# Kernel optimization log

Hardware: AMD Instinct MI355X
Metric: run time of the kernel (lower is better)

Reference implementation:

```python
import jax, jax.numpy as jnp
import numpy as np


def _conv1x1(w, x):
    # w: [out, in], x: [B, in, H, W] -> [B, out, H, W]
    return jnp.einsum('oc,bchw->bohw', w, x)


def _maxpool2(x):
    # 2x2 max pool, stride 2. x: [B, C, H, W] -> [B, C, H//2, W//2]
    B, C, H, W = x.shape
    return x.reshape(B, C, H // 2, 2, W // 2, 2).max(axis=(3, 5))


def setup_inputs() -> dict:
    key = jax.random.key(0)
    ks = jax.random.split(key, 5)
    B, C, H, W = 8, 256, 64, 64
    div = 8
    x = jax.random.normal(ks[0], (B, C, H, W), dtype=jnp.float32)
    wq = jax.random.normal(ks[1], (C // div, C), dtype=jnp.float32) * (C ** -0.5)
    wk = jax.random.normal(ks[2], (C // div, C), dtype=jnp.float32) * (C ** -0.5)
    wv = jax.random.normal(ks[3], (C // 2, C), dtype=jnp.float32) * (C ** -0.5)
    wo = jax.random.normal(ks[4], (C, C // 2), dtype=jnp.float32) * ((C // 2) ** -0.5)
    gamma = jnp.float32(0.5)  # nonzero so attention branch contributes
    return {"x": x, "wq": wq, "wk": wk, "wv": wv, "wo": wo, "gamma": gamma}


def reference(x, wq, wk, wv, wo, gamma):
    B, C, H, W = x.shape
    HW = H * W
    # query: [B, HW, Cq]
    q = _conv1x1(wq, x).reshape(B, -1, HW).transpose(0, 2, 1)
    # key: maxpool -> [B, Cq, HW//4]
    k = _maxpool2(_conv1x1(wk, x)).reshape(B, -1, HW // 4)
    # value: maxpool -> [B, C//2, HW//4]
    v = _maxpool2(_conv1x1(wv, x)).reshape(B, -1, HW // 4)
    scores = jnp.einsum('bnc,bcm->bnm', q, k)          # [B, HW, HW//4]
    attn = jax.nn.softmax(scores, axis=2)
    ctx = jnp.einsum('bcm,bnm->bcn', v, attn)          # [B, C//2, HW]
    ctx = ctx.reshape(B, C // 2, H, W)
    out = gamma * _conv1x1(wo, ctx) + x
    return out
```

## Files before the change

kernel.cpp:

```cpp
#include <hip/hip_runtime.h>
#include <hip/hip_bf16.h>

#define BB  8
#define CC  256
#define HW  4096
#define CQ  32
#define CV  128
#define MP  1024

#define XT_OFF  0
#define Y_OFF   4194304
#define KT_OFF  (Y_OFF + 3145728)
#define VP_OFF  (KT_OFF + 131072)
#define CT_OFF  (VP_OFF + 524288)
#define P0_OFF  CT_OFF
#define P1_OFF  XT_OFF
#define ML_OFF  (XT_OFF + 2097152)

typedef __attribute__((ext_vector_type(8))) short bf16x8;
typedef __attribute__((ext_vector_type(4))) short short4v;
typedef __attribute__((ext_vector_type(4))) float f32x4;

__device__ __forceinline__ short f2b(float f) {
    unsigned u = __float_as_uint(f);
    u += 0x7fffu + ((u >> 16) & 1u);
    return (short)(u >> 16);
}
__device__ __forceinline__ float b2f(short s) {
    return __uint_as_float(((unsigned)(unsigned short)s) << 16);
}

__global__ __launch_bounds__(256) void k_xt(
    const float* __restrict__ x, short* __restrict__ xt)
{
    __shared__ float t[64][65];
    const int bid = blockIdx.x;
    const int nt = bid & 63;
    const int ct = (bid >> 6) & 3;
    const int b  = bid >> 8;
    const int c0 = ct * 64, n0 = nt * 64;
    const int tid = threadIdx.x;

    const int col = tid & 63, wrow = (tid >> 6) * 16;
    #pragma unroll
    for (int i = 0; i < 16; ++i) {
        int r = wrow + i;
        t[r][col] = x[((long)(b * CC + c0 + r)) * HW + n0 + col];
    }
    __syncthreads();

    const int n = tid >> 2, cb = (tid & 3) * 16;
    short buf[16];
    #pragma unroll
    for (int j = 0; j < 16; ++j) buf[j] = f2b(t[cb + j][n]);
    short* dst = &xt[((long)(b * HW + n0 + n)) * CC + c0 + cb];
    *(int4*)dst = *(int4*)&buf[0];
    *(int4*)(dst + 8) = *(int4*)&buf[8];
}

__global__ __launch_bounds__(256) void k_qkv(
    const float* __restrict__ wq, const float* __restrict__ wk,
    const float* __restrict__ wv, const short* __restrict__ xt,
    short* __restrict__ y)
{
    __shared__ short w_lds[96 * 264];
    __shared__ short x_lds[256 * 40];
    const int bid = blockIdx.x;
    const int oc = bid & 1;
    const int nt = (bid >> 1) & 15;
    const int b  = bid >> 5;
    const int o0 = oc * 96, n0 = nt * 256;
    const int tid = threadIdx.x;
    const int lane = tid & 63;
    const int wvid = tid >> 6;
    const int l15 = lane & 15, g = lane >> 4;

    for (int it = 0; it < 24; ++it) {
        int idx = tid + it * 256;
        int ol = idx >> 6, cq = (idx & 63) * 4;
        int o = o0 + ol;
        const float* src = (o < 32) ? &wq[o * 256 + cq]
                         : (o < 64) ? &wk[(o - 32) * 256 + cq]
                                    : &wv[(o - 64) * 256 + cq];
        float4 w = *(const float4*)src;
        short4v p = { f2b(w.x), f2b(w.y), f2b(w.z), f2b(w.w) };
        *(short4v*)&w_lds[ol * 264 + cq] = p;
    }

    f32x4 acc[4][6];
    #pragma unroll
    for (int nf = 0; nf < 4; ++nf)
        #pragma unroll
        for (int of = 0; of < 6; ++of) acc[nf][of] = (f32x4){0.f, 0.f, 0.f, 0.f};

    for (int ks = 0; ks < 8; ++ks) {
        __syncthreads();
        {
            const short* src = &xt[((long)(b * HW + n0 + tid)) * CC + ks * 32];
            int4 v0 = *(const int4*)src;
            int4 v1 = *(const int4*)(src + 8);
            int4 v2 = *(const int4*)(src + 16);
            int4 v3 = *(const int4*)(src + 24);
            short* dst = &x_lds[tid * 40];
            *(int4*)dst = v0; *(int4*)(dst + 8) = v1;
            *(int4*)(dst + 16) = v2; *(int4*)(dst + 24) = v3;
        }
        __syncthreads();

        bf16x8 a[4], bf[6];
        #pragma unroll
        for (int nf = 0; nf < 4; ++nf)
            a[nf] = *(const bf16x8*)&x_lds[(wvid * 64 + nf * 16 + l15) * 40 + 8 * g];
        #pragma unroll
        for (int of = 0; of < 6; ++of)
            bf[of] = *(const bf16x8*)&w_lds[(of * 16 + l15) * 264 + ks * 32 + 8 * g];
        #pragma unroll
        for (int nf = 0; nf < 4; ++nf)
            #pragma unroll
            for (int of = 0; of < 6; ++of)
                acc[nf][of] = __builtin_amdgcn_mfma_f32_16x16x32_bf16(a[nf], bf[of], acc[nf][of], 0, 0, 0);
    }

    #pragma unroll
    for (int nf = 0; nf < 4; ++nf) {
        #pragma unroll
        for (int of = 0; of < 6; ++of) {
            int o = o0 + of * 16 + l15;
            long nb = (long)(b * HW + n0 + wvid * 64 + nf * 16 + 4 * g);
            #pragma unroll
            for (int r = 0; r < 4; ++r)
                y[(nb + r) * 192 + o] = f2b(acc[nf][of][r]);
        }
    }
}

__global__ __launch_bounds__(256) void k_pool(
    const short* __restrict__ y, short* __restrict__ kT, short* __restrict__ vp)
{
    __shared__ short t[64 * 136];
    const int bid = blockIdx.x;
    const int mt = bid & 15;
    const int b  = bid >> 4;
    const int m0 = mt * 64;
    const int tid = threadIdx.x;

    {
        int ml = tid >> 2, ci = (tid & 3) * 8;
        int pp = m0 + ml;
        int ph = pp >> 5, pw = pp & 31;
        const short* src = &y[((long)(b * HW) + ph * 128 + pw * 2) * 192 + 32 + ci];
        int4 s0 = *(const int4*)src;
        int4 s1 = *(const int4*)(src + 192);
        int4 s2 = *(const int4*)(src + 12288);
        int4 s3 = *(const int4*)(src + 12480);
        const short *a = (const short*)&s0, *bb = (const short*)&s1,
                    *c = (const short*)&s2, *d = (const short*)&s3;
        short o8[8];
        #pragma unroll
        for (int j = 0; j < 8; ++j)
            o8[j] = f2b(fmaxf(fmaxf(b2f(a[j]), b2f(bb[j])), fmaxf(b2f(c[j]), b2f(d[j]))));
        *(int4*)&kT[((long)(b * MP + pp)) * CQ + ci] = *(int4*)o8;
    }
    #pragma unroll
    for (int jj = 0; jj < 4; ++jj) {
        int idx = tid + jj * 256;
        int ml = idx >> 4, ci = (idx & 15) * 8;
        int pp = m0 + ml;
        int ph = pp >> 5, pw = pp & 31;
        const short* src = &y[((long)(b * HW) + ph * 128 + pw * 2) * 192 + 64 + ci];
        int4 s0 = *(const int4*)src;
        int4 s1 = *(const int4*)(src + 192);
        int4 s2 = *(const int4*)(src + 12288);
        int4 s3 = *(const int4*)(src + 12480);
        const short *a = (const short*)&s0, *bb = (const short*)&s1,
                    *c = (const short*)&s2, *d = (const short*)&s3;
        short o8[8];
        #pragma unroll
        for (int j = 0; j < 8; ++j)
            o8[j] = f2b(fmaxf(fmaxf(b2f(a[j]), b2f(bb[j])), fmaxf(b2f(c[j]), b2f(d[j]))));
        *(int4*)&t[ml * 136 + ci] = *(int4*)o8;
    }
    __syncthreads();
    {
        int c = tid & 127, mc = (tid >> 7) * 32;
        short buf[32];
        #pragma unroll
        for (int mm = 0; mm < 32; ++mm) buf[mm] = t[(mc + mm) * 136 + c];
        short* dst = &vp[((long)(b * CV + c)) * MP + m0 + mc];
        *(int4*)dst = *(int4*)&buf[0];
        *(int4*)(dst + 8)  = *(int4*)&buf[8];
        *(int4*)(dst + 16) = *(int4*)&buf[16];
        *(int4*)(dst + 24) = *(int4*)&buf[24];
    }
}

__global__ __launch_bounds__(128) void k_attn(
    const short* __restrict__ y,
    const short* __restrict__ kT,
    const short* __restrict__ vp,
    short* __restrict__ p0,
    short* __restrict__ p1,
    float* __restrict__ ml)
{
    __shared__ short p_lds[2][2][16][40];
    const int tid   = threadIdx.x;
    const int lane  = tid & 63;
    const int wid   = tid >> 6;
    const int split = blockIdx.x >> 9;
    const int rem   = blockIdx.x & 511;
    const int b     = rem >> 6;
    const int q0    = (rem & 63) * 64 + wid * 32;
    const int l15   = lane & 15;
    const int g     = lane >> 4;

    bf16x8 qf[2];
    const short* yq = y + (long)b * HW * 192;
    #pragma unroll
    for (int si = 0; si < 2; ++si)
        qf[si] = *(const bf16x8*)&yq[(long)(q0 + si * 16 + l15) * 192 + 8 * g];

    float m_run[2] = {-INFINITY, -INFINITY};
    float l_run[2] = {0.f, 0.f};
    f32x4 acc[2][8];
    #pragma unroll
    for (int si = 0; si < 2; ++si)
        #pragma unroll
        for (int ct = 0; ct < 8; ++ct)
            acc[si][ct] = (f32x4){0.f, 0.f, 0.f, 0.f};

    const short* kTb = kT + (long)b * MP * CQ;
    const short* vpb = vp + (long)b * CV * MP;

    for (int mt = 0; mt < 16; ++mt) {
        const int m0 = split * 512 + mt * 32;
        bf16x8 ka0 = *(const bf16x8*)&kTb[(m0 + l15) * CQ + 8 * g];
        bf16x8 ka1 = *(const bf16x8*)&kTb[(m0 + 16 + l15) * CQ + 8 * g];
        bf16x8 va[8];
        #pragma unroll
        for (int ct = 0; ct < 8; ++ct)
            va[ct] = *(const bf16x8*)&vpb[(ct * 16 + l15) * MP + m0 + 8 * g];

        #pragma unroll
        for (int si = 0; si < 2; ++si) {
            f32x4 s0 = (f32x4){0.f, 0.f, 0.f, 0.f};
            f32x4 s1 = (f32x4){0.f, 0.f, 0.f, 0.f};
            s0 = __builtin_amdgcn_mfma_f32_16x16x32_bf16(ka0, qf[si], s0, 0, 0, 0);
            s1 = __builtin_amdgcn_mfma_f32_16x16x32_bf16(ka1, qf[si], s1, 0, 0, 0);
            float tmax8 = fmaxf(fmaxf(fmaxf(s0[0], s0[1]), fmaxf(s0[2], s0[3])),
                                fmaxf(fmaxf(s1[0], s1[1]), fmaxf(s1[2], s1[3])));
            float mr = m_run[si];
            if (!__all(tmax8 <= mr + 8.0f)) {
                float tmax = fmaxf(tmax8, __shfl_xor(tmax8, 16, 64));
                tmax = fmaxf(tmax, __shfl_xor(tmax, 32, 64));
                float nm    = fmaxf(mr, tmax);
                float alpha = __expf(mr - nm);
                l_run[si] *= alpha;
                #pragma unroll
                for (int r = 0; r < 4; ++r) {
                    float ar = __shfl(alpha, 4 * g + r, 64);
                    #pragma unroll
                    for (int ct = 0; ct < 8; ++ct) acc[si][ct][r] *= ar;
                }
                m_run[si] = nm;
                mr = nm;
            }
            float p[8];
            #pragma unroll
            for (int r = 0; r < 4; ++r) { p[r] = __expf(s0[r] - mr); p[4 + r] = __expf(s1[r] - mr); }
            l_run[si] += ((p[0] + p[1]) + (p[2] + p[3])) + ((p[4] + p[5]) + (p[6] + p[7]));
            short4v w0 = { f2b(p[0]), f2b(p[1]), f2b(p[2]), f2b(p[3]) };
            short4v w1 = { f2b(p[4]), f2b(p[5]), f2b(p[6]), f2b(p[7]) };
            *(short4v*)&p_lds[wid][si][l15][4 * g]      = w0;
            *(short4v*)&p_lds[wid][si][l15][16 + 4 * g] = w1;
        }
        #pragma unroll
        for (int si = 0; si < 2; ++si) {
            bf16x8 pf = *(const bf16x8*)&p_lds[wid][si][l15][8 * g];
            #pragma unroll
            for (int ct = 0; ct < 8; ++ct)
                acc[si][ct] = __builtin_amdgcn_mfma_f32_16x16x32_bf16(pf, va[ct], acc[si][ct], 0, 0, 0);
        }
    }

    #pragma unroll
    for (int si = 0; si < 2; ++si) {
        l_run[si] += __shfl_xor(l_run[si], 16, 64);
        l_run[si] += __shfl_xor(l_run[si], 32, 64);
    }

    short* pp = split ? p1 : p0;
    #pragma unroll
    for (int si = 0; si < 2; ++si) {
        float inv = 1.f / l_run[si];
        #pragma unroll
        for (int r = 0; r < 4; ++r) {
            float invr = __shfl(inv, 4 * g + r, 64);
            long q = q0 + si * 16 + 4 * g + r;
            short* cb = &pp[((long)b * HW + q) * CV];
            #pragma unroll
            for (int ct = 0; ct < 8; ++ct)
                cb[ct * 16 + l15] = f2b(acc[si][ct][r] * invr);
        }
    }
    if (lane < 16) {
        #pragma unroll
        for (int si = 0; si < 2; ++si) {
            long row = (long)(split * BB + b) * HW + q0 + si * 16 + lane;
            ml[row * 2]     = m_run[si];
            ml[row * 2 + 1] = l_run[si];
        }
    }
}

__global__ __launch_bounds__(256) void k_comb(
    const short* __restrict__ p0, const short* __restrict__ p1,
    const float* __restrict__ ml, short* __restrict__ ctx)
{
    const long idx = (long)blockIdx.x * 256 + threadIdx.x;
    const long row = idx >> 4;
    const int  c0  = (int)(idx & 15) * 8;
    const float m0 = ml[row * 2],                      l0 = ml[row * 2 + 1];
    const float m1 = ml[((long)BB * HW + row) * 2],    l1 = ml[((long)BB * HW + row) * 2 + 1];
    const float M  = fmaxf(m0, m1);
    float w0 = l0 * __expf(m0 - M);
    float w1 = l1 * __expf(m1 - M);
    const float inv = 1.f / (w0 + w1);
    w0 *= inv; w1 *= inv;
    int4 a4 = *(const int4*)&p0[row * CV + c0];
    int4 b4 = *(const int4*)&p1[row * CV + c0];
    const short* as = (const short*)&a4;
    const short* bs = (const short*)&b4;
    short o8[8];
    #pragma unroll
    for (int j = 0; j < 8; ++j)
        o8[j] = f2b(w0 * b2f(as[j]) + w1 * b2f(bs[j]));
    *(int4*)&ctx[row * CV + c0] = *(int4*)o8;
}

__global__ __launch_bounds__(256) void k_out(
    const short* __restrict__ ctx, const float* __restrict__ wo,
    const float* __restrict__ x, const float* __restrict__ gamma,
    float* __restrict__ out)
{
    __shared__ short c_lds[256 * 136];
    __shared__ short w_lds[128 * 136];
    const int bid = blockIdx.x;
    const int oc = bid & 1;
    const int nt = (bid >> 1) & 15;
    const int b  = bid >> 5;
    const int o0 = oc * 128, n0 = nt * 256;
    const int tid = threadIdx.x;
    const int lane = tid & 63;
    const int l15 = lane & 15, g = lane >> 4;

    {
        const short* src = &ctx[((long)(b * HW + n0 + tid)) * CV];
        short* dst = &c_lds[tid * 136];
        #pragma unroll
        for (int j = 0; j < 16; ++j)
            *(int4*)(dst + 8 * j) = *(const int4*)(src + 8 * j);
    }
    for (int it = 0; it < 16; ++it) {
        int idx = tid + it * 256;
        int ol = idx >> 5, cq = (idx & 31) * 4;
        float4 w = *(const float4*)&wo[(o0 + ol) * CV + cq];
        short4v p = { f2b(w.x), f2b(w.y), f2b(w.z), f2b(w.w) };
        *(short4v*)&w_lds[ol * 136 + cq] = p;
    }
    __syncthreads();

    const int wvid = tid >> 6;
    const int ow = (wvid & 1) * 64, nw = (wvid >> 1) * 128;
    f32x4 acc[4][8];
    #pragma unroll
    for (int of = 0; of < 4; ++of)
        #pragma unroll
        for (int nf = 0; nf < 8; ++nf) acc[of][nf] = (f32x4){0.f, 0.f, 0.f, 0.f};

    #pragma unroll
    for (int ks = 0; ks < 4; ++ks) {
        bf16x8 af[4], bf[8];
        #pragma unroll
        for (int of = 0; of < 4; ++of)
            af[of] = *(const bf16x8*)&w_lds[(ow + of * 16 + l15) * 136 + ks * 32 + 8 * g];
        #pragma unroll
        for (int nf = 0; nf < 8; ++nf)
            bf[nf] = *(const bf16x8*)&c_lds[(nw + nf * 16 + l15) * 136 + ks * 32 + 8 * g];
        #pragma unroll
        for (int of = 0; of < 4; ++of)
            #pragma unroll
            for (int nf = 0; nf < 8; ++nf)
                acc[of][nf] = __builtin_amdgcn_mfma_f32_16x16x32_bf16(af[of], bf[nf], acc[of][nf], 0, 0, 0);
    }

    const float gma = gamma[0];
    #pragma unroll
    for (int of = 0; of < 4; ++of) {
        #pragma unroll
        for (int r = 0; r < 4; ++r) {
            int o = o0 + ow + of * 16 + 4 * g + r;
            #pragma unroll
            for (int nf = 0; nf < 8; ++nf) {
                int n = n0 + nw + nf * 16 + l15;
                long idx = (long)(b * CC + o) * HW + n;
                out[idx] = gma * acc[of][nf][r] + x[idx];
            }
        }
    }
}

extern "C" void kernel_launch(void* const* d_in, const int* in_sizes, int n_in,
                              void* d_out, int out_size, void* d_ws, size_t ws_size,
                              hipStream_t stream) {
    const float* x     = (const float*)d_in[0];
    const float* wq    = (const float*)d_in[1];
    const float* wk    = (const float*)d_in[2];
    const float* wv    = (const float*)d_in[3];
    const float* wo    = (const float*)d_in[4];
    const float* gamma = (const float*)d_in[5];
    float* out = (float*)d_out;
    float* ws  = (float*)d_ws;

    short* xt  = (short*)(ws + XT_OFF);
    short* y   = (short*)(ws + Y_OFF);
    short* kT  = (short*)(ws + KT_OFF);
    short* vp  = (short*)(ws + VP_OFF);
    short* ctx = (short*)(ws + CT_OFF);
    short* p0  = (short*)(ws + P0_OFF);
    short* p1  = (short*)(ws + P1_OFF);
    float* mlb = ws + ML_OFF;

    k_xt  <<<dim3(2048), dim3(256), 0, stream>>>(x, xt);
    k_qkv <<<dim3(256),  dim3(256), 0, stream>>>(wq, wk, wv, xt, y);
    k_pool<<<dim3(128),  dim3(256), 0, stream>>>(y, kT, vp);
    k_attn<<<dim3(1024), dim3(128), 0, stream>>>(y, kT, vp, p0, p1, mlb);
    k_comb<<<dim3(2048), dim3(256), 0, stream>>>(p0, p1, mlb, ctx);
    k_out <<<dim3(256),  dim3(256), 0, stream>>>(ctx, wo, x, gamma, out);
}
```

Baseline: 96.39 us.

## Split attention KV range four ways and use output buffer for partials

The attention kernel now splits the 1024 pooled keys into four chunks of 256 instead of two, doubling the grid to 2048 blocks so more waves can be resident and latency is better hidden. The three extra bf16 partial-context buffers are placed in the output buffer, which is free until the final kernel. The max/sum stats move into the no-longer-needed transposed-x region. The combine kernel merges four partials with log-sum-exp weights. In exchange it writes and reads twice as much partial-context data, and the combine step does more work.

```diff
diff --git a/kernel.cpp b/kernel.cpp
--- a/kernel.cpp
+++ b/kernel.cpp
@@ -14,8 +14,7 @@
 #define VP_OFF  (KT_OFF + 131072)
 #define CT_OFF  (VP_OFF + 524288)
 #define P0_OFF  CT_OFF
-#define P1_OFF  XT_OFF
-#define ML_OFF  (XT_OFF + 2097152)
+#define ML_OFF  XT_OFF
 
 typedef __attribute__((ext_vector_type(8))) short bf16x8;
 typedef __attribute__((ext_vector_type(4))) short short4v;
@@ -199,7 +198,7 @@
     const short* __restrict__ kT,
     const short* __restrict__ vp,
     short* __restrict__ p0,
-    short* __restrict__ p1,
+    short* __restrict__ p1b,
     float* __restrict__ ml)
 {
     __shared__ short p_lds[2][2][16][40];
@@ -231,8 +230,8 @@
     const short* kTb = kT + (long)b * MP * CQ;
     const short* vpb = vp + (long)b * CV * MP;
 
-    for (int mt = 0; mt < 16; ++mt) {
-        const int m0 = split * 512 + mt * 32;
+    for (int mt = 0; mt < 8; ++mt) {
+        const int m0 = split * 256 + mt * 32;
         bf16x8 ka0 = *(const bf16x8*)&kTb[(m0 + l15) * CQ + 8 * g];
         bf16x8 ka1 = *(const bf16x8*)&kTb[(m0 + 16 + l15) * CQ + 8 * g];
         bf16x8 va[8];
@@ -288,7 +287,7 @@
         l_run[si] += __shfl_xor(l_run[si], 32, 64);
     }
 
-    short* pp = split ? p1 : p0;
+    short* pp = (split == 0) ? p0 : p1b + (long)(split - 1) * ((long)BB * HW * CV);
     #pragma unroll
     for (int si = 0; si < 2; ++si) {
         float inv = 1.f / l_run[si];
@@ -313,27 +312,41 @@
 }
 
 __global__ __launch_bounds__(256) void k_comb(
-    const short* __restrict__ p0, const short* __restrict__ p1,
+    const short* __restrict__ p0, const short* __restrict__ p1b,
     const float* __restrict__ ml, short* __restrict__ ctx)
 {
     const long idx = (long)blockIdx.x * 256 + threadIdx.x;
     const long row = idx >> 4;
     const int  c0  = (int)(idx & 15) * 8;
-    const float m0 = ml[row * 2],                      l0 = ml[row * 2 + 1];
-    const float m1 = ml[((long)BB * HW + row) * 2],    l1 = ml[((long)BB * HW + row) * 2 + 1];
-    const float M  = fmaxf(m0, m1);
-    float w0 = l0 * __expf(m0 - M);
-    float w1 = l1 * __expf(m1 - M);
-    const float inv = 1.f / (w0 + w1);
-    w0 *= inv; w1 *= inv;
-    int4 a4 = *(const int4*)&p0[row * CV + c0];
-    int4 b4 = *(const int4*)&p1[row * CV + c0];
-    const short* as = (const short*)&a4;
-    const short* bs = (const short*)&b4;
+    const long NR  = (long)BB * HW;
+
+    float m[4], l[4];
+    #pragma unroll
+    for (int s = 0; s < 4; ++s) {
+        m[s] = ml[(s * NR + row) * 2];
+        l[s] = ml[(s * NR + row) * 2 + 1];
+    }
+    float M = fmaxf(fmaxf(m[0], m[1]), fmaxf(m[2], m[3]));
+    float w[4], wsum = 0.f;
+    #pragma unroll
+    for (int s = 0; s < 4; ++s) { w[s] = l[s] * __expf(m[s] - M); wsum += w[s]; }
+    const float inv = 1.f / wsum;
+
+    int4 v[4];
+    v[0] = *(const int4*)&p0[row * CV + c0];
+    #pragma unroll
+    for (int s = 1; s < 4; ++s)
+        v[s] = *(const int4*)&p1b[(long)(s - 1) * (NR * CV) + row * CV + c0];
+
     short o8[8];
     #pragma unroll
-    for (int j = 0; j < 8; ++j)
-        o8[j] = f2b(w0 * b2f(as[j]) + w1 * b2f(bs[j]));
+    for (int j = 0; j < 8; ++j) {
+        float acc = 0.f;
+        #pragma unroll
+        for (int s = 0; s < 4; ++s)
+            acc += w[s] * b2f(((const short*)&v[s])[j]);
+        o8[j] = f2b(acc * inv);
+    }
     *(int4*)&ctx[row * CV + c0] = *(int4*)o8;
 }
 
@@ -427,13 +440,13 @@
     short* vp  = (short*)(ws + VP_OFF);
     short* ctx = (short*)(ws + CT_OFF);
     short* p0  = (short*)(ws + P0_OFF);
-    short* p1  = (short*)(ws + P1_OFF);
+    short* p1b = (short*)d_out;
     float* mlb = ws + ML_OFF;
 
     k_xt  <<<dim3(2048), dim3(256), 0, stream>>>(x, xt);
     k_qkv <<<dim3(256),  dim3(256), 0, stream>>>(wq, wk, wv, xt, y);
     k_pool<<<dim3(128),  dim3(256), 0, stream>>>(y, kT, vp);
-    k_attn<<<dim3(1024), dim3(128), 0, stream>>>(y, kT, vp, p0, p1, mlb);
-    k_comb<<<dim3(2048), dim3(256), 0, stream>>>(p0, p1, mlb, ctx);
+    k_attn<<<dim3(2048), dim3(128), 0, stream>>>(y, kT, vp, p0, p1b, mlb);
+    k_comb<<<dim3(2048), dim3(256), 0, stream>>>(p0, p1b, mlb, ctx);
     k_out <<<dim3(256),  dim3(256), 0, stream>>>(ctx, wo, x, gamma, out);
 }
```

After: 101.5 us. +5.3%, slower.

## Fuse split-softmax combine into output projection and prefetch K/V tiles in attention

Applied to the files above, without the earlier changes.

The separate combine kernel that merged the two attention split partials into a ctx buffer is removed. Its rescale-and-sum now runs inside the output-projection kernel while it loads into LDS, which saves one launch and a full write and read of ctx. The attention loop also software-pipelines its global loads of K and V fragments one tile ahead, trying to hide load latency behind the MFMA work. The cost is more register pressure from holding two sets of V fragments, which could lower occupancy.

```diff
diff --git a/kernel.cpp b/kernel.cpp
--- a/kernel.cpp
+++ b/kernel.cpp
@@ -230,15 +230,23 @@
 
     const short* kTb = kT + (long)b * MP * CQ;
     const short* vpb = vp + (long)b * CV * MP;
+    const int mbase = split * 512;
+
+    bf16x8 ka0 = *(const bf16x8*)&kTb[(mbase + l15) * CQ + 8 * g];
+    bf16x8 ka1 = *(const bf16x8*)&kTb[(mbase + 16 + l15) * CQ + 8 * g];
+    bf16x8 va[8];
+    #pragma unroll
+    for (int ct = 0; ct < 8; ++ct)
+        va[ct] = *(const bf16x8*)&vpb[(ct * 16 + l15) * MP + mbase + 8 * g];
 
     for (int mt = 0; mt < 16; ++mt) {
-        const int m0 = split * 512 + mt * 32;
-        bf16x8 ka0 = *(const bf16x8*)&kTb[(m0 + l15) * CQ + 8 * g];
-        bf16x8 ka1 = *(const bf16x8*)&kTb[(m0 + 16 + l15) * CQ + 8 * g];
-        bf16x8 va[8];
+        const int mn = mbase + (mt < 15 ? mt + 1 : mt) * 32;
+        bf16x8 ka0n = *(const bf16x8*)&kTb[(mn + l15) * CQ + 8 * g];
+        bf16x8 ka1n = *(const bf16x8*)&kTb[(mn + 16 + l15) * CQ + 8 * g];
+        bf16x8 van[8];
         #pragma unroll
         for (int ct = 0; ct < 8; ++ct)
-            va[ct] = *(const bf16x8*)&vpb[(ct * 16 + l15) * MP + m0 + 8 * g];
+            van[ct] = *(const bf16x8*)&vpb[(ct * 16 + l15) * MP + mn + 8 * g];
 
         #pragma unroll
         for (int si = 0; si < 2; ++si) {
@@ -280,6 +288,9 @@
             for (int ct = 0; ct < 8; ++ct)
                 acc[si][ct] = __builtin_amdgcn_mfma_f32_16x16x32_bf16(pf, va[ct], acc[si][ct], 0, 0, 0);
         }
+        ka0 = ka0n; ka1 = ka1n;
+        #pragma unroll
+        for (int ct = 0; ct < 8; ++ct) va[ct] = van[ct];
     }
 
     #pragma unroll
@@ -312,33 +323,9 @@
     }
 }
 
-__global__ __launch_bounds__(256) void k_comb(
+__global__ __launch_bounds__(256) void k_out(
     const short* __restrict__ p0, const short* __restrict__ p1,
-    const float* __restrict__ ml, short* __restrict__ ctx)
-{
-    const long idx = (long)blockIdx.x * 256 + threadIdx.x;
-    const long row = idx >> 4;
-    const int  c0  = (int)(idx & 15) * 8;
-    const float m0 = ml[row * 2],                      l0 = ml[row * 2 + 1];
-    const float m1 = ml[((long)BB * HW + row) * 2],    l1 = ml[((long)BB * HW + row) * 2 + 1];
-    const float M  = fmaxf(m0, m1);
-    float w0 = l0 * __expf(m0 - M);
-    float w1 = l1 * __expf(m1 - M);
-    const float inv = 1.f / (w0 + w1);
-    w0 *= inv; w1 *= inv;
-    int4 a4 = *(const int4*)&p0[row * CV + c0];
-    int4 b4 = *(const int4*)&p1[row * CV + c0];
-    const short* as = (const short*)&a4;
-    const short* bs = (const short*)&b4;
-    short o8[8];
-    #pragma unroll
-    for (int j = 0; j < 8; ++j)
-        o8[j] = f2b(w0 * b2f(as[j]) + w1 * b2f(bs[j]));
-    *(int4*)&ctx[row * CV + c0] = *(int4*)o8;
-}
-
-__global__ __launch_bounds__(256) void k_out(
-    const short* __restrict__ ctx, const float* __restrict__ wo,
+    const float* __restrict__ ml, const float* __restrict__ wo,
     const float* __restrict__ x, const float* __restrict__ gamma,
     float* __restrict__ out)
 {
@@ -352,13 +339,31 @@
     const int tid = threadIdx.x;
     const int lane = tid & 63;
     const int l15 = lane & 15, g = lane >> 4;
+    const long NR = (long)BB * HW;
 
     {
-        const short* src = &ctx[((long)(b * HW + n0 + tid)) * CV];
+        const long grow = (long)(b * HW + n0 + tid);
+        const float m0v = ml[grow * 2],        l0v = ml[grow * 2 + 1];
+        const float m1v = ml[(NR + grow) * 2], l1v = ml[(NR + grow) * 2 + 1];
+        const float M = fmaxf(m0v, m1v);
+        float w0 = l0v * __expf(m0v - M);
+        float w1 = l1v * __expf(m1v - M);
+        const float inv = 1.f / (w0 + w1);
+        w0 *= inv; w1 *= inv;
+        const short* s0 = &p0[grow * CV];
+        const short* s1 = &p1[grow * CV];
         short* dst = &c_lds[tid * 136];
         #pragma unroll
-        for (int j = 0; j < 16; ++j)
-            *(int4*)(dst + 8 * j) = *(const int4*)(src + 8 * j);
+        for (int j = 0; j < 16; ++j) {
+            int4 a4 = *(const int4*)(s0 + 8 * j);
+            int4 b4 = *(const int4*)(s1 + 8 * j);
+            short o8[8];
+            #pragma unroll
+            for (int k = 0; k < 8; ++k)
+                o8[k] = f2b(w0 * b2f(((const short*)&a4)[k])
+                          + w1 * b2f(((const short*)&b4)[k]));
+            *(int4*)(dst + 8 * j) = *(int4*)o8;
+        }
     }
     for (int it = 0; it < 16; ++it) {
         int idx = tid + it * 256;
@@ -425,7 +430,6 @@
     short* y   = (short*)(ws + Y_OFF);
     short* kT  = (short*)(ws + KT_OFF);
     short* vp  = (short*)(ws + VP_OFF);
-    short* ctx = (short*)(ws + CT_OFF);
     short* p0  = (short*)(ws + P0_OFF);
     short* p1  = (short*)(ws + P1_OFF);
     float* mlb = ws + ML_OFF;
@@ -434,6 +438,5 @@
     k_qkv <<<dim3(256),  dim3(256), 0, stream>>>(wq, wk, wv, xt, y);
     k_pool<<<dim3(128),  dim3(256), 0, stream>>>(y, kT, vp);
     k_attn<<<dim3(1024), dim3(128), 0, stream>>>(y, kT, vp, p0, p1, mlb);
-    k_comb<<<dim3(2048), dim3(256), 0, stream>>>(p0, p1, mlb, ctx);
-    k_out <<<dim3(256),  dim3(256), 0, stream>>>(ctx, wo, x, gamma, out);
-}
+    k_out <<<dim3(256),  dim3(256), 0, stream>>>(p0, p1, mlb, wo, x, gamma, out);
+}
```

After: 99.17 us. +2.9%, slower.
